# Kernel optimization log

Measured on AMD Instinct MI355X. Metric: run time of the kernel, lower is better.

## Reference

```python
import jax, jax.numpy as jnp
import numpy as np

B, C, L = 4, 192, 4096
DIV = 3
CO = C // DIV  # 64


def setup_inputs() -> dict:
    key = jax.random.key(0)
    ks = jax.random.split(key, 6)
    # kaiming-normal-ish init for 1x1 conv weights, stored as (out, in) matrices
    std = float(np.sqrt(2.0 / C))
    return {
        "x": jax.random.normal(ks[0], (B, C, L, 1), dtype=jnp.float32),
        "Wq": jax.random.normal(ks[1], (CO, C), dtype=jnp.float32) * std,
        "Wk": jax.random.normal(ks[2], (CO, C), dtype=jnp.float32) * std,
        "Wv": jax.random.normal(ks[3], (CO, C), dtype=jnp.float32) * std,
        "Wv1": jax.random.normal(ks[4], (CO, C), dtype=jnp.float32) * std,
        "gamma": jnp.zeros((1,), dtype=jnp.float32) + 0.5,  # nonzero so attn path is exercised
    }


def reference(x, Wq, Wk, Wv, Wv1, gamma):
    b, c, l, _ = x.shape
    xf = x.reshape(b, c, l)                      # (B, C, L)
    f = jnp.einsum("oc,bcl->bol", Wq, xf)        # (B, CO, L)
    g = jnp.einsum("oc,bcl->bol", Wk, xf)
    h = jnp.einsum("oc,bcl->bol", Wv, xf)
    v1 = jnp.einsum("oc,bcl->bol", Wv1, xf)
    # scores[b, l, m] = sum_o f[b,o,l] * g[b,o,m]; softmax over dim=1 (l axis)
    scores = jnp.einsum("bol,bom->blm", f, g)    # (B, L, L)
    beta = jax.nn.softmax(scores, axis=1)
    o = gamma * jnp.einsum("bol,blm->bom", h, beta) + v1  # (B, CO, L)
    return o.reshape(b, c // 3, l, 1)
```

## Files before the change

kernel.cpp:

```cpp
#include <hip/hip_runtime.h>
#include <math.h>

#define B_ 4
#define C_ 192
#define L_ 4096
#define CO_ 64
#define LOG2E 1.44269504088896340736f

using half8 = __attribute__((ext_vector_type(8))) _Float16;
using half4v = __attribute__((ext_vector_type(4))) _Float16;
using half2v = __attribute__((ext_vector_type(2))) _Float16;
using f32x16 = __attribute__((ext_vector_type(16))) float;

#if __has_builtin(__builtin_amdgcn_exp2f)
#define EXP2(x) __builtin_amdgcn_exp2f(x)
#else
#define EXP2(x) exp2f(x)
#endif

__device__ inline half2v pkrtz(float a, float b) {
  return __builtin_bit_cast(half2v, __builtin_amdgcn_cvt_pkrtz(a, b));
}


__global__ __launch_bounds__(256) void wpack_kernel(
    const float* __restrict__ Wq, const float* __restrict__ Wk,
    const float* __restrict__ Wv, const float* __restrict__ Wv1,
    _Float16* __restrict__ Wpack) {
  const int tid = blockIdx.x * 256 + threadIdx.x;
  const int w = tid / 1536;
  const int rem = tid % 1536;
  const int og = rem / 768;
  const int ks = (rem % 768) / 64;
  const int lane = rem % 64;
  const float* src = (w == 0) ? Wq : (w == 1) ? Wk : (w == 2) ? Wv : Wv1;
  const float s = (w == 0) ? LOG2E : 1.0f;
  const int row = og * 32 + (lane & 31);
  const int col = ks * 16 + (lane >> 5) * 8;
  const float* p = src + row * C_ + col;
  const float4 a = *(const float4*)(p);
  const float4 c = *(const float4*)(p + 4);
  half8 o;
  half2v t;
  t = pkrtz(a.x * s, a.y * s); o[0] = t[0]; o[1] = t[1];
  t = pkrtz(a.z * s, a.w * s); o[2] = t[0]; o[3] = t[1];
  t = pkrtz(c.x * s, c.y * s); o[4] = t[0]; o[5] = t[1];
  t = pkrtz(c.z * s, c.w * s); o[6] = t[0]; o[7] = t[1];
  *(half8*)(Wpack + (size_t)tid * 8) = o;
}

__global__ __launch_bounds__(256) void proj_mfma(
    const float* __restrict__ x, const _Float16* __restrict__ Wpack,
    _Float16* __restrict__ fPack, _Float16* __restrict__ gB,
    _Float16* __restrict__ hPack, float* __restrict__ v1N) {
  __shared__ __align__(16) float xs[C_ * 32];
  __shared__ __align__(16) _Float16 fl[32 * 72];
  __shared__ __align__(16) _Float16 hl[64 * 40];
  const int b = blockIdx.y, T = blockIdx.x, l0 = T * 32;
  const int t = threadIdx.x;
  const int lane = t & 63, w = t >> 6;
  const int m = lane & 31, hi = lane >> 5;

  {
    const float* xb = x + (size_t)b * C_ * L_ + l0;
    const int c0 = w * 48;
#pragma unroll
    for (int i = 0; i < 6; ++i) {
      const int cc = c0 + i * 8;
      const float* gp = xb + (size_t)(cc + (lane >> 3)) * L_ + (lane & 7) * 4;
      __builtin_amdgcn_global_load_lds(
          (const __attribute__((address_space(1))) void*)gp,
          (__attribute__((address_space(3))) void*)&xs[cc * 32], 16, 0, 0);
    }
  }
  __syncthreads();

  const _Float16* Wp = Wpack + (size_t)w * 1536 * 8;
  half8 wf[2][12];
#pragma unroll
  for (int og = 0; og < 2; ++og)
#pragma unroll
    for (int ks = 0; ks < 12; ++ks)
      wf[og][ks] = *(const half8*)(Wp + ((size_t)(og * 12 + ks) * 64 + lane) * 8);

  if (w < 2) {
    f32x16 acc0 = {}, acc1 = {};
#pragma unroll
    for (int ks = 0; ks < 12; ++ks) {
      const float* xr = &xs[(ks * 16 + hi * 8) * 32 + m];
      half8 aF;
#pragma unroll
      for (int e = 0; e < 8; e += 2) {
        const half2v hp = pkrtz(xr[e * 32], xr[(e + 1) * 32]);
        aF[e] = hp[0]; aF[e + 1] = hp[1];
      }
      acc0 = __builtin_amdgcn_mfma_f32_32x32x16_f16(aF, wf[0][ks], acc0, 0, 0, 0);
      acc1 = __builtin_amdgcn_mfma_f32_32x32x16_f16(aF, wf[1][ks], acc1, 0, 0, 0);
    }
    if (w == 0) {
#pragma unroll
      for (int r = 0; r < 16; ++r) {
        const int l = 4 * hi + 8 * (r >> 2) + (r & 3);
        fl[l * 72 + m] = (_Float16)acc0[r];
        fl[l * 72 + 32 + m] = (_Float16)acc1[r];
      }
      _Float16* dst = fPack + (size_t)b * L_ * CO_ + (size_t)T * 4 * 64 * 8;
#pragma unroll
      for (int ks = 0; ks < 4; ++ks) {
        const half8 v = *(const half8*)&fl[(lane & 31) * 72 + ks * 16 + (lane >> 5) * 8];
        *(half8*)(dst + ((size_t)ks * 64 + lane) * 8) = v;
      }
    } else {
      _Float16* dst = gB;
#pragma unroll
      for (int r = 0; r < 16; ++r) {
        const int lrow = 4 * hi + 8 * (r >> 2) + (r & 3);
        _Float16* row = dst + ((size_t)b * L_ + l0 + lrow) * CO_;
        row[m] = (_Float16)acc0[r];
        row[32 + m] = (_Float16)acc1[r];
      }
    }
  } else {
    const int lg = l0 + m;
    for (int oh = 0; oh < 2; ++oh) {
      f32x16 acc = {};
#pragma unroll
      for (int ks = 0; ks < 12; ++ks) {
        const float* xr = &xs[(16 * ks + 8 * hi) * 32 + m];
        half8 bF;
#pragma unroll
        for (int e = 0; e < 8; e += 2) {
          const half2v hp = pkrtz(xr[e * 32], xr[(e + 1) * 32]);
          bF[e] = hp[0]; bF[e + 1] = hp[1];
        }
        acc = __builtin_amdgcn_mfma_f32_32x32x16_f16(wf[oh][ks], bF, acc, 0, 0, 0);
      }
      if (w == 2) {
#pragma unroll
        for (int r = 0; r < 16; ++r) {
          const int o = 32 * oh + 4 * hi + 8 * (r >> 2) + (r & 3);
          hl[o * 40 + m] = (_Float16)acc[r];
        }
      } else {
#pragma unroll
        for (int r = 0; r < 16; ++r) {
          const int o = 32 * oh + 4 * hi + 8 * (r >> 2) + (r & 3);
          v1N[((size_t)b * CO_ + o) * L_ + lg] = acc[r];
        }
      }
    }
    if (w == 2) {
      _Float16* dst = hPack + (size_t)b * L_ * CO_ + (size_t)T * 4 * 64 * 8;
#pragma unroll
      for (int j = 0; j < 4; ++j) {
        const int oh2 = j >> 1, ks2 = j & 1;
        const half8 v = *(const half8*)&hl[(32 * oh2 + (lane & 31)) * 40 +
                                           ks2 * 16 + (lane >> 5) * 8];
        *(half8*)(dst + ((size_t)j * 64 + lane) * 8) = v;
      }
    }
  }
}

__device__ __forceinline__ void softmax_o(const f32x16& S, float& mx, float& Z,
                                          f32x16& oa, f32x16& ob,
                                          const half8* hc, _Float16* Pw,
                                          int m, int hi) {
  float tmax = S[0];
#pragma unroll
  for (int r = 1; r < 16; ++r) tmax = fmaxf(tmax, S[r]);
  tmax = fmaxf(tmax, __shfl_xor(tmax, 32, 64));
  if (__any(tmax > mx)) {
    const float mnew = fmaxf(mx, tmax);
    const float corr = EXP2(mx - mnew);
    mx = mnew;
    Z *= corr;
#pragma unroll
    for (int r = 0; r < 16; ++r) { oa[r] *= corr; ob[r] *= corr; }
  }
  float zl = 0.f;
#pragma unroll
  for (int u = 0; u < 4; ++u) {
    const float p0 = EXP2(S[4 * u + 0] - mx);
    const float p1 = EXP2(S[4 * u + 1] - mx);
    const float p2 = EXP2(S[4 * u + 2] - mx);
    const float p3 = EXP2(S[4 * u + 3] - mx);
    zl += (p0 + p1) + (p2 + p3);
    const half2v lo = pkrtz(p0, p1);
    const half2v hi2 = pkrtz(p2, p3);
    half4v w4; w4[0] = lo[0]; w4[1] = lo[1]; w4[2] = hi2[0]; w4[3] = hi2[1];
    *(half4v*)(Pw + m * 40 + 4 * hi + 8 * u) = w4;
  }
  Z += zl;
  const half8 bP0 = *(const half8*)(Pw + m * 40 + 8 * hi);
  const half8 bP1 = *(const half8*)(Pw + m * 40 + 16 + 8 * hi);
  oa = __builtin_amdgcn_mfma_f32_32x32x16_f16(hc[0], bP0, oa, 0, 0, 0);
  oa = __builtin_amdgcn_mfma_f32_32x32x16_f16(hc[1], bP1, oa, 0, 0, 0);
  ob = __builtin_amdgcn_mfma_f32_32x32x16_f16(hc[2], bP0, ob, 0, 0, 0);
  ob = __builtin_amdgcn_mfma_f32_32x32x16_f16(hc[3], bP1, ob, 0, 0, 0);
}

__global__ __launch_bounds__(512, 2) void attn_mfma(
    const _Float16* __restrict__ fPack, const _Float16* __restrict__ gB,
    const _Float16* __restrict__ hPack, const float* __restrict__ v1N,
    const float* __restrict__ gamma_p, float* __restrict__ out) {
  __shared__ __align__(16) _Float16 Pl[8][32 * 40];
  __shared__ float obuf4[4][CO_][65];
  __shared__ float redM[8][64];
  __shared__ float redZ[8][64];

  const int id = blockIdx.x;
  const int b = (id >> 1) & 3;
  const int mt = ((id & 1) << 5) | (id >> 3);
  const int m0 = mt * 64;
  const int t = threadIdx.x;
  const int lane = t & 63, s = t >> 6;
  const int m = lane & 31, hi = lane >> 5;

  const _Float16* fT = fPack + (size_t)b * L_ * CO_;
  const _Float16* hT = hPack + (size_t)b * L_ * CO_;
  _Float16* Pw = &Pl[s][0];

  const _Float16* g0 = gB + ((size_t)b * L_ + m0 + m) * CO_ + hi * 8;
  const _Float16* g1 = g0 + (size_t)32 * CO_;
  half8 gf0[4], gf1[4];
#pragma unroll
  for (int ks = 0; ks < 4; ++ks) {
    gf0[ks] = *(const half8*)(g0 + ks * 16);
    gf1[ks] = *(const half8*)(g1 + ks * 16);
  }

  f32x16 o0 = {}, o1 = {}, o2 = {}, o3 = {};
  float mx0 = -1e30f, Z0 = 0.f, mx1 = -1e30f, Z1 = 0.f;

  const int T0 = s * 16;
  half8 fc[2][4], hc[2][4];
  {
    const _Float16* fp = fT + ((size_t)T0 * 4 * 64 + lane) * 8;
    const _Float16* hp = hT + ((size_t)T0 * 4 * 64 + lane) * 8;
#pragma unroll
    for (int ks = 0; ks < 4; ++ks) {
      fc[0][ks] = *(const half8*)(fp + (size_t)ks * 64 * 8);
      hc[0][ks] = *(const half8*)(hp + (size_t)ks * 64 * 8);
    }
  }

#pragma unroll 2
  for (int stp = 0; stp < 16; ++stp) {
    const int cur = stp & 1, nxt = cur ^ 1;
    {
      const int Tn = T0 + stp + 1;
      const _Float16* fp = fT + ((size_t)Tn * 4 * 64 + lane) * 8;
      const _Float16* hp = hT + ((size_t)Tn * 4 * 64 + lane) * 8;
#pragma unroll
      for (int ks = 0; ks < 4; ++ks) {
        fc[nxt][ks] = *(const half8*)(fp + (size_t)ks * 64 * 8);
        hc[nxt][ks] = *(const half8*)(hp + (size_t)ks * 64 * 8);
      }
    }
    f32x16 S0 = {}, S1 = {};
#pragma unroll
    for (int ks = 0; ks < 4; ++ks) {
      S0 = __builtin_amdgcn_mfma_f32_32x32x16_f16(fc[cur][ks], gf0[ks], S0, 0, 0, 0);
      S1 = __builtin_amdgcn_mfma_f32_32x32x16_f16(fc[cur][ks], gf1[ks], S1, 0, 0, 0);
    }
    softmax_o(S0, mx0, Z0, o0, o1, hc[cur], Pw, m, hi);
    softmax_o(S1, mx1, Z1, o2, o3, hc[cur], Pw, m, hi);
  }

  Z0 += __shfl_xor(Z0, 32, 64);
  Z1 += __shfl_xor(Z1, 32, 64);
  if (hi == 0) {
    redM[s][m] = mx0; redM[s][m + 32] = mx1;
    redZ[s][m] = Z0;  redZ[s][m + 32] = Z1;
  }
  __syncthreads();
  float M0 = redM[0][m], M1 = redM[0][m + 32];
#pragma unroll
  for (int i = 1; i < 8; ++i) {
    M0 = fmaxf(M0, redM[i][m]);
    M1 = fmaxf(M1, redM[i][m + 32]);
  }
  const float sc0 = EXP2(mx0 - M0);
  const float sc1 = EXP2(mx1 - M1);
  if (s < 4) {
#pragma unroll
    for (int r = 0; r < 16; ++r) {
      const int o = 4 * hi + 8 * (r >> 2) + (r & 3);
      obuf4[s][o][m] = sc0 * o0[r];
      obuf4[s][o + 32][m] = sc0 * o1[r];
      obuf4[s][o][m + 32] = sc1 * o2[r];
      obuf4[s][o + 32][m + 32] = sc1 * o3[r];
    }
  }
  __syncthreads();
  if (s >= 4) {
#pragma unroll
    for (int r = 0; r < 16; ++r) {
      const int o = 4 * hi + 8 * (r >> 2) + (r & 3);
      obuf4[s - 4][o][m] += sc0 * o0[r];
      obuf4[s - 4][o + 32][m] += sc0 * o1[r];
      obuf4[s - 4][o][m + 32] += sc1 * o2[r];
      obuf4[s - 4][o + 32][m + 32] += sc1 * o3[r];
    }
  }
  __syncthreads();

  const float gam = gamma_p[0];
  const int me = t & 63;
  const int og = t >> 6;
  float M = redM[0][me];
#pragma unroll
  for (int i = 1; i < 8; ++i) M = fmaxf(M, redM[i][me]);
  float Zt = 0.f;
#pragma unroll
  for (int i = 0; i < 8; ++i) Zt += EXP2(redM[i][me] - M) * redZ[i][me];
  const float inv = 1.0f / Zt;
#pragma unroll
  for (int i = 0; i < 8; ++i) {
    const int o = og * 8 + i;
    const float val = obuf4[0][o][me] + obuf4[1][o][me] +
                      obuf4[2][o][me] + obuf4[3][o][me];
    const size_t g = ((size_t)b * CO_ + o) * L_ + m0 + me;
    out[g] = gam * val * inv + v1N[g];
  }
}

extern "C" void kernel_launch(void* const* d_in, const int* in_sizes, int n_in,
                              void* d_out, int out_size, void* d_ws,
                              size_t ws_size, hipStream_t stream) {
  const float* x = (const float*)d_in[0];
  const float* Wq = (const float*)d_in[1];
  const float* Wk = (const float*)d_in[2];
  const float* Wv = (const float*)d_in[3];
  const float* Wv1 = (const float*)d_in[4];
  const float* gamma = (const float*)d_in[5];
  float* out = (float*)d_out;

  _Float16* Wpack = (_Float16*)d_ws;
  _Float16* fPack = Wpack + (size_t)4 * 1536 * 8;
  _Float16* gB = fPack + (size_t)B_ * L_ * CO_;
  _Float16* hPack = gB + (size_t)B_ * L_ * CO_;
  float* v1N = (float*)(hPack + (size_t)B_ * L_ * CO_);

  wpack_kernel<<<24, 256, 0, stream>>>(Wq, Wk, Wv, Wv1, Wpack);
  proj_mfma<<<dim3(L_ / 32, B_), 256, 0, stream>>>(x, Wpack, fPack, gB, hPack, v1N);
  attn_mfma<<<256, 512, 0, stream>>>(fPack, gB, hPack, v1N, gamma, out);
}
```

Before: 105.6 us.

## Fuse weight packing into projection, pack g layout, interleave dual softmax tiles

Removes the separate weight-packing kernel: each projection wave now loads its fp32 weight rows directly and converts them to fp16 fragments in registers, overlapping with the async x load. The g projection is written in the same packed fragment layout as f, so the attention kernel loads it with coalesced half8 reads. The attention inner loop now processes both 32-column score tiles together, with a single wave-vote rescale branch, interleaved exp work, and a larger P staging buffer so the eight output MFMAs can be issued back to back. This saves a launch and gives more instruction-level parallelism, at the cost of redundant weight conversion in every projection block, more LDS, and more register pressure.

```diff
diff --git a/kernel.cpp b/kernel.cpp
--- a/kernel.cpp
+++ b/kernel.cpp
@@ -23,38 +23,15 @@
 }
 
 
-__global__ __launch_bounds__(256) void wpack_kernel(
-    const float* __restrict__ Wq, const float* __restrict__ Wk,
-    const float* __restrict__ Wv, const float* __restrict__ Wv1,
-    _Float16* __restrict__ Wpack) {
-  const int tid = blockIdx.x * 256 + threadIdx.x;
-  const int w = tid / 1536;
-  const int rem = tid % 1536;
-  const int og = rem / 768;
-  const int ks = (rem % 768) / 64;
-  const int lane = rem % 64;
-  const float* src = (w == 0) ? Wq : (w == 1) ? Wk : (w == 2) ? Wv : Wv1;
-  const float s = (w == 0) ? LOG2E : 1.0f;
-  const int row = og * 32 + (lane & 31);
-  const int col = ks * 16 + (lane >> 5) * 8;
-  const float* p = src + row * C_ + col;
-  const float4 a = *(const float4*)(p);
-  const float4 c = *(const float4*)(p + 4);
-  half8 o;
-  half2v t;
-  t = pkrtz(a.x * s, a.y * s); o[0] = t[0]; o[1] = t[1];
-  t = pkrtz(a.z * s, a.w * s); o[2] = t[0]; o[3] = t[1];
-  t = pkrtz(c.x * s, c.y * s); o[4] = t[0]; o[5] = t[1];
-  t = pkrtz(c.z * s, c.w * s); o[6] = t[0]; o[7] = t[1];
-  *(half8*)(Wpack + (size_t)tid * 8) = o;
-}
-
 __global__ __launch_bounds__(256) void proj_mfma(
-    const float* __restrict__ x, const _Float16* __restrict__ Wpack,
-    _Float16* __restrict__ fPack, _Float16* __restrict__ gB,
-    _Float16* __restrict__ hPack, float* __restrict__ v1N) {
+    const float* __restrict__ x, const float* __restrict__ Wq,
+    const float* __restrict__ Wk, const float* __restrict__ Wv,
+    const float* __restrict__ Wv1, _Float16* __restrict__ fPack,
+    _Float16* __restrict__ gPack, _Float16* __restrict__ hPack,
+    float* __restrict__ v1N) {
   __shared__ __align__(16) float xs[C_ * 32];
   __shared__ __align__(16) _Float16 fl[32 * 72];
+  __shared__ __align__(16) _Float16 gl[32 * 72];
   __shared__ __align__(16) _Float16 hl[64 * 40];
   const int b = blockIdx.y, T = blockIdx.x, l0 = T * 32;
   const int t = threadIdx.x;
@@ -73,15 +50,24 @@
           (__attribute__((address_space(3))) void*)&xs[cc * 32], 16, 0, 0);
     }
   }
+
+  const float* Wsrc = (w == 0) ? Wq : (w == 1) ? Wk : (w == 2) ? Wv : Wv1;
+  const float ws = (w == 0) ? LOG2E : 1.0f;
+  half8 wf[2][12];
+#pragma unroll
+  for (int og = 0; og < 2; ++og)
+#pragma unroll
+    for (int ks = 0; ks < 12; ++ks) {
+      const float* p = Wsrc + (og * 32 + m) * C_ + ks * 16 + hi * 8;
+      const float4 a = *(const float4*)p;
+      const float4 c = *(const float4*)(p + 4);
+      half2v h;
+      h = pkrtz(a.x * ws, a.y * ws); wf[og][ks][0] = h[0]; wf[og][ks][1] = h[1];
+      h = pkrtz(a.z * ws, a.w * ws); wf[og][ks][2] = h[0]; wf[og][ks][3] = h[1];
+      h = pkrtz(c.x * ws, c.y * ws); wf[og][ks][4] = h[0]; wf[og][ks][5] = h[1];
+      h = pkrtz(c.z * ws, c.w * ws); wf[og][ks][6] = h[0]; wf[og][ks][7] = h[1];
+    }
   __syncthreads();
-
-  const _Float16* Wp = Wpack + (size_t)w * 1536 * 8;
-  half8 wf[2][12];
-#pragma unroll
-  for (int og = 0; og < 2; ++og)
-#pragma unroll
-    for (int ks = 0; ks < 12; ++ks)
-      wf[og][ks] = *(const half8*)(Wp + ((size_t)(og * 12 + ks) * 64 + lane) * 8);
 
   if (w < 2) {
     f32x16 acc0 = {}, acc1 = {};
@@ -97,28 +83,20 @@
       acc0 = __builtin_amdgcn_mfma_f32_32x32x16_f16(aF, wf[0][ks], acc0, 0, 0, 0);
       acc1 = __builtin_amdgcn_mfma_f32_32x32x16_f16(aF, wf[1][ks], acc1, 0, 0, 0);
     }
-    if (w == 0) {
-#pragma unroll
-      for (int r = 0; r < 16; ++r) {
-        const int l = 4 * hi + 8 * (r >> 2) + (r & 3);
-        fl[l * 72 + m] = (_Float16)acc0[r];
-        fl[l * 72 + 32 + m] = (_Float16)acc1[r];
-      }
-      _Float16* dst = fPack + (size_t)b * L_ * CO_ + (size_t)T * 4 * 64 * 8;
-#pragma unroll
-      for (int ks = 0; ks < 4; ++ks) {
-        const half8 v = *(const half8*)&fl[(lane & 31) * 72 + ks * 16 + (lane >> 5) * 8];
-        *(half8*)(dst + ((size_t)ks * 64 + lane) * 8) = v;
-      }
-    } else {
-      _Float16* dst = gB;
-#pragma unroll
-      for (int r = 0; r < 16; ++r) {
-        const int lrow = 4 * hi + 8 * (r >> 2) + (r & 3);
-        _Float16* row = dst + ((size_t)b * L_ + l0 + lrow) * CO_;
-        row[m] = (_Float16)acc0[r];
-        row[32 + m] = (_Float16)acc1[r];
-      }
+    _Float16* buf = (w == 0) ? fl : gl;
+#pragma unroll
+    for (int r = 0; r < 16; ++r) {
+      const int l = 4 * hi + 8 * (r >> 2) + (r & 3);
+      buf[l * 72 + m] = (_Float16)acc0[r];
+      buf[l * 72 + 32 + m] = (_Float16)acc1[r];
+    }
+    _Float16* dst = ((w == 0) ? fPack : gPack) +
+                    (size_t)b * L_ * CO_ + (size_t)T * 4 * 64 * 8;
+#pragma unroll
+    for (int ks = 0; ks < 4; ++ks) {
+      const half8 v =
+          *(const half8*)&buf[(lane & 31) * 72 + ks * 16 + (lane >> 5) * 8];
+      *(half8*)(dst + ((size_t)ks * 64 + lane) * 8) = v;
     }
   } else {
     const int lg = l0 + m;
@@ -162,49 +140,11 @@
   }
 }
 
-__device__ __forceinline__ void softmax_o(const f32x16& S, float& mx, float& Z,
-                                          f32x16& oa, f32x16& ob,
-                                          const half8* hc, _Float16* Pw,
-                                          int m, int hi) {
-  float tmax = S[0];
-#pragma unroll
-  for (int r = 1; r < 16; ++r) tmax = fmaxf(tmax, S[r]);
-  tmax = fmaxf(tmax, __shfl_xor(tmax, 32, 64));
-  if (__any(tmax > mx)) {
-    const float mnew = fmaxf(mx, tmax);
-    const float corr = EXP2(mx - mnew);
-    mx = mnew;
-    Z *= corr;
-#pragma unroll
-    for (int r = 0; r < 16; ++r) { oa[r] *= corr; ob[r] *= corr; }
-  }
-  float zl = 0.f;
-#pragma unroll
-  for (int u = 0; u < 4; ++u) {
-    const float p0 = EXP2(S[4 * u + 0] - mx);
-    const float p1 = EXP2(S[4 * u + 1] - mx);
-    const float p2 = EXP2(S[4 * u + 2] - mx);
-    const float p3 = EXP2(S[4 * u + 3] - mx);
-    zl += (p0 + p1) + (p2 + p3);
-    const half2v lo = pkrtz(p0, p1);
-    const half2v hi2 = pkrtz(p2, p3);
-    half4v w4; w4[0] = lo[0]; w4[1] = lo[1]; w4[2] = hi2[0]; w4[3] = hi2[1];
-    *(half4v*)(Pw + m * 40 + 4 * hi + 8 * u) = w4;
-  }
-  Z += zl;
-  const half8 bP0 = *(const half8*)(Pw + m * 40 + 8 * hi);
-  const half8 bP1 = *(const half8*)(Pw + m * 40 + 16 + 8 * hi);
-  oa = __builtin_amdgcn_mfma_f32_32x32x16_f16(hc[0], bP0, oa, 0, 0, 0);
-  oa = __builtin_amdgcn_mfma_f32_32x32x16_f16(hc[1], bP1, oa, 0, 0, 0);
-  ob = __builtin_amdgcn_mfma_f32_32x32x16_f16(hc[2], bP0, ob, 0, 0, 0);
-  ob = __builtin_amdgcn_mfma_f32_32x32x16_f16(hc[3], bP1, ob, 0, 0, 0);
-}
-
 __global__ __launch_bounds__(512, 2) void attn_mfma(
-    const _Float16* __restrict__ fPack, const _Float16* __restrict__ gB,
+    const _Float16* __restrict__ fPack, const _Float16* __restrict__ gPack,
     const _Float16* __restrict__ hPack, const float* __restrict__ v1N,
     const float* __restrict__ gamma_p, float* __restrict__ out) {
-  __shared__ __align__(16) _Float16 Pl[8][32 * 40];
+  __shared__ __align__(16) _Float16 Pl[8][64 * 40];
   __shared__ float obuf4[4][CO_][65];
   __shared__ float redM[8][64];
   __shared__ float redZ[8][64];
@@ -221,13 +161,15 @@
   const _Float16* hT = hPack + (size_t)b * L_ * CO_;
   _Float16* Pw = &Pl[s][0];
 
-  const _Float16* g0 = gB + ((size_t)b * L_ + m0 + m) * CO_ + hi * 8;
-  const _Float16* g1 = g0 + (size_t)32 * CO_;
   half8 gf0[4], gf1[4];
-#pragma unroll
-  for (int ks = 0; ks < 4; ++ks) {
-    gf0[ks] = *(const half8*)(g0 + ks * 16);
-    gf1[ks] = *(const half8*)(g1 + ks * 16);
+  {
+    const _Float16* gp = gPack + (size_t)b * L_ * CO_ +
+                         (size_t)(2 * mt) * 4 * 64 * 8 + lane * 8;
+#pragma unroll
+    for (int ks = 0; ks < 4; ++ks) {
+      gf0[ks] = *(const half8*)(gp + (size_t)ks * 64 * 8);
+      gf1[ks] = *(const half8*)(gp + (size_t)(4 + ks) * 64 * 8);
+    }
   }
 
   f32x16 o0 = {}, o1 = {}, o2 = {}, o3 = {};
@@ -264,8 +206,60 @@
       S0 = __builtin_amdgcn_mfma_f32_32x32x16_f16(fc[cur][ks], gf0[ks], S0, 0, 0, 0);
       S1 = __builtin_amdgcn_mfma_f32_32x32x16_f16(fc[cur][ks], gf1[ks], S1, 0, 0, 0);
     }
-    softmax_o(S0, mx0, Z0, o0, o1, hc[cur], Pw, m, hi);
-    softmax_o(S1, mx1, Z1, o2, o3, hc[cur], Pw, m, hi);
+    float t0 = S0[0], t1 = S1[0];
+#pragma unroll
+    for (int r = 1; r < 16; ++r) {
+      t0 = fmaxf(t0, S0[r]);
+      t1 = fmaxf(t1, S1[r]);
+    }
+    t0 = fmaxf(t0, __shfl_xor(t0, 32, 64));
+    t1 = fmaxf(t1, __shfl_xor(t1, 32, 64));
+    if (__any(t0 > mx0 || t1 > mx1)) {
+      const float mn0 = fmaxf(mx0, t0), mn1 = fmaxf(mx1, t1);
+      const float c0 = EXP2(mx0 - mn0), c1 = EXP2(mx1 - mn1);
+      mx0 = mn0; mx1 = mn1;
+      Z0 *= c0; Z1 *= c1;
+#pragma unroll
+      for (int r = 0; r < 16; ++r) {
+        o0[r] *= c0; o1[r] *= c0;
+        o2[r] *= c1; o3[r] *= c1;
+      }
+    }
+    float zl0 = 0.f, zl1 = 0.f;
+#pragma unroll
+    for (int u = 0; u < 4; ++u) {
+      const float a0 = EXP2(S0[4 * u + 0] - mx0);
+      const float a1 = EXP2(S0[4 * u + 1] - mx0);
+      const float a2 = EXP2(S0[4 * u + 2] - mx0);
+      const float a3 = EXP2(S0[4 * u + 3] - mx0);
+      zl0 += (a0 + a1) + (a2 + a3);
+      const half2v lo = pkrtz(a0, a1);
+      const half2v hi2 = pkrtz(a2, a3);
+      half4v w4; w4[0] = lo[0]; w4[1] = lo[1]; w4[2] = hi2[0]; w4[3] = hi2[1];
+      *(half4v*)(Pw + m * 40 + 4 * hi + 8 * u) = w4;
+      const float b0 = EXP2(S1[4 * u + 0] - mx1);
+      const float b1 = EXP2(S1[4 * u + 1] - mx1);
+      const float b2 = EXP2(S1[4 * u + 2] - mx1);
+      const float b3 = EXP2(S1[4 * u + 3] - mx1);
+      zl1 += (b0 + b1) + (b2 + b3);
+      const half2v lo2 = pkrtz(b0, b1);
+      const half2v hi3 = pkrtz(b2, b3);
+      half4v w5; w5[0] = lo2[0]; w5[1] = lo2[1]; w5[2] = hi3[0]; w5[3] = hi3[1];
+      *(half4v*)(Pw + (32 + m) * 40 + 4 * hi + 8 * u) = w5;
+    }
+    Z0 += zl0; Z1 += zl1;
+    const half8 bP0 = *(const half8*)(Pw + m * 40 + 8 * hi);
+    const half8 bP1 = *(const half8*)(Pw + m * 40 + 16 + 8 * hi);
+    const half8 bQ0 = *(const half8*)(Pw + (32 + m) * 40 + 8 * hi);
+    const half8 bQ1 = *(const half8*)(Pw + (32 + m) * 40 + 16 + 8 * hi);
+    o0 = __builtin_amdgcn_mfma_f32_32x32x16_f16(hc[cur][0], bP0, o0, 0, 0, 0);
+    o1 = __builtin_amdgcn_mfma_f32_32x32x16_f16(hc[cur][2], bP0, o1, 0, 0, 0);
+    o2 = __builtin_amdgcn_mfma_f32_32x32x16_f16(hc[cur][0], bQ0, o2, 0, 0, 0);
+    o3 = __builtin_amdgcn_mfma_f32_32x32x16_f16(hc[cur][2], bQ0, o3, 0, 0, 0);
+    o0 = __builtin_amdgcn_mfma_f32_32x32x16_f16(hc[cur][1], bP1, o0, 0, 0, 0);
+    o1 = __builtin_amdgcn_mfma_f32_32x32x16_f16(hc[cur][3], bP1, o1, 0, 0, 0);
+    o2 = __builtin_amdgcn_mfma_f32_32x32x16_f16(hc[cur][1], bQ1, o2, 0, 0, 0);
+    o3 = __builtin_amdgcn_mfma_f32_32x32x16_f16(hc[cur][3], bQ1, o3, 0, 0, 0);
   }
 
   Z0 += __shfl_xor(Z0, 32, 64);
@@ -337,13 +331,12 @@
   const float* gamma = (const float*)d_in[5];
   float* out = (float*)d_out;
 
-  _Float16* Wpack = (_Float16*)d_ws;
-  _Float16* fPack = Wpack + (size_t)4 * 1536 * 8;
-  _Float16* gB = fPack + (size_t)B_ * L_ * CO_;
-  _Float16* hPack = gB + (size_t)B_ * L_ * CO_;
+  _Float16* fPack = (_Float16*)d_ws;
+  _Float16* gPack = fPack + (size_t)B_ * L_ * CO_;
+  _Float16* hPack = gPack + (size_t)B_ * L_ * CO_;
   float* v1N = (float*)(hPack + (size_t)B_ * L_ * CO_);
 
-  wpack_kernel<<<24, 256, 0, stream>>>(Wq, Wk, Wv, Wv1, Wpack);
-  proj_mfma<<<dim3(L_ / 32, B_), 256, 0, stream>>>(x, Wpack, fPack, gB, hPack, v1N);
-  attn_mfma<<<256, 512, 0, stream>>>(fPack, gB, hPack, v1N, gamma, out);
+  proj_mfma<<<dim3(L_ / 32, B_), 256, 0, stream>>>(x, Wq, Wk, Wv, Wv1, fPack,
+                                                   gPack, hPack, v1N);
+  attn_mfma<<<256, 512, 0, stream>>>(fPack, gPack, hPack, v1N, gamma, out);
 }
```

Measured after the change: 111.3 us. +5.4%, slower.
